# Kernel optimization log

Measured on AMD Instinct MI355X. Metric: run time of the kernel, lower is better.

The kernel has to match this reference:

```python
import jax, jax.numpy as jnp
import numpy as np

B, N, D, S = 16, 128, 128, 128   # batch, n_nodes, node/edge feat dim, state_dim
MP_INT = 256
UP_INT = 256
EPS = 1e-3  # keras BatchNormalization default epsilon


def _mlp(x, W1, b1, W2, b2):
    # Dense(relu) -> Dense(relu)
    h = jax.nn.relu(x @ W1 + b1)
    return jax.nn.relu(h @ W2 + b2)


def setup_inputs() -> dict:
    key = jax.random.key(0)
    ks = jax.random.split(key, 16)
    g = lambda k, shape: jax.random.normal(k, shape, dtype=jnp.float32) * 0.05
    nodes = jax.random.normal(ks[0], (B, N, D), dtype=jnp.float32)
    edges = jax.random.normal(ks[1], (B, N * N, D), dtype=jnp.float32)
    mask = (jax.random.uniform(ks[2], (B, N * N, 1)) > 0.5).astype(jnp.float32)
    return {
        "nodes": nodes, "edges": edges, "mask": mask,
        # Adj_Updater_1: concat(node_i, node_j, edge_ij) -> UP_INT -> S
        "W1a": g(ks[3], (3 * D, UP_INT)), "b1a": jnp.zeros((UP_INT,), jnp.float32),
        "W2a": g(ks[4], (UP_INT, S)), "b2a": jnp.zeros((S,), jnp.float32),
        # Message_Passer_1: concat(node_i, node_j, new_edge) -> MP_INT -> S
        "W1m": g(ks[5], (2 * D + S, MP_INT)), "b1m": jnp.zeros((MP_INT,), jnp.float32),
        "W2m": g(ks[6], (MP_INT, S)), "b2m": jnp.zeros((S,), jnp.float32),
        # Update_Func_1: concat(old_state, agg_messages) -> UP_INT -> S
        "W1u": g(ks[7], (D + S, UP_INT)), "b1u": jnp.zeros((UP_INT,), jnp.float32),
        "W2u": g(ks[8], (UP_INT, S)), "b2u": jnp.zeros((S,), jnp.float32),
        # BatchNorm (inference mode: moving stats) for nodes and edges
        "gamma_n": jnp.ones((S,), jnp.float32), "beta_n": jnp.zeros((S,), jnp.float32),
        "mean_n": jnp.zeros((S,), jnp.float32), "var_n": jnp.ones((S,), jnp.float32),
        "gamma_e": jnp.ones((S,), jnp.float32), "beta_e": jnp.zeros((S,), jnp.float32),
        "mean_e": jnp.zeros((S,), jnp.float32), "var_e": jnp.ones((S,), jnp.float32),
    }


def reference(nodes, edges, mask,
              W1a, b1a, W2a, b2a,
              W1m, b1m, W2m, b2m,
              W1u, b1u, W2u, b2u,
              gamma_n, beta_n, mean_n, var_n,
              gamma_e, beta_e, mean_e, var_e):
    b, n, d = nodes.shape
    # tf.tile(nodes,[1,n,1]): row p*n+q -> nodes[q]  (state_i)
    state_i = jnp.broadcast_to(nodes[:, None, :, :], (b, n, n, d)).reshape(b, n * n, d)
    # reshape(tile(nodes,[1,1,n])): row p*n+q -> nodes[p]  (state_j)
    state_j = jnp.broadcast_to(nodes[:, :, None, :], (b, n, n, d)).reshape(b, n * n, d)

    new_edges = _mlp(jnp.concatenate([state_i, state_j, edges], axis=-1), W1a, b1a, W2a, b2a)
    new_edges = new_edges * mask

    messages = _mlp(jnp.concatenate([state_i, state_j, new_edges], axis=-1), W1m, b1m, W2m, b2m)
    masked = (messages * mask).reshape(b, n, n, -1)
    agg_m = masked.sum(axis=2)  # reduce over axis 2 as in Message_Agg

    state_1 = _mlp(jnp.concatenate([nodes, agg_m], axis=-1), W1u, b1u, W2u, b2u)

    bn = lambda x, g_, b_, m_, v_: g_ * (x - m_) * jax.lax.rsqrt(v_ + EPS) + b_
    nodes_out = bn(state_1, gamma_n, beta_n, mean_n, var_n)
    edges_out = bn(new_edges, gamma_e, beta_e, mean_e, var_e)
    return nodes_out, edges_out
```

## Files before the change

### kernel.cpp

```cpp
#include <hip/hip_runtime.h>
#include <hip/hip_bf16.h>
#include <cstdint>
#include <cstddef>


typedef __attribute__((ext_vector_type(8))) __bf16 bf16x8;
typedef __attribute__((ext_vector_type(4))) float f32x4;

#define GLDS(gp, lp)                                                        \
  __builtin_amdgcn_global_load_lds(                                         \
      (const __attribute__((address_space(1))) void*)(gp),                  \
      (__attribute__((address_space(3))) void*)(lp), 16, 0, 0)

__device__ inline bf16x8 load8_cvt(const float* __restrict__ p) {
  const float4 a = *(const float4*)p;
  const float4 b = *(const float4*)(p + 4);
  bf16x8 r;
  r[0] = (__bf16)a.x; r[1] = (__bf16)a.y; r[2] = (__bf16)a.z; r[3] = (__bf16)a.w;
  r[4] = (__bf16)b.x; r[5] = (__bf16)b.y; r[6] = (__bf16)b.z; r[7] = (__bf16)b.w;
  return r;
}

__global__ void __launch_bounds__(256) proj_kernel(
    const float* __restrict__ nodes, const float* __restrict__ W1a,
    const float* __restrict__ b1a, const float* __restrict__ W1m,
    const float* __restrict__ b1m, const float* __restrict__ ge,
    const float* __restrict__ be, const float* __restrict__ me,
    const float* __restrict__ ve, float* __restrict__ outP) {
  __shared__ float x[8][128];
  const int mat = blockIdx.y;
  const int t = threadIdx.x;
  const float* W = (mat < 2 ? W1a : W1m) + ((mat & 1) ? 128 * 256 : 0);
  float* out = outP + (size_t)mat * (2048 * 256);
  const int r0 = blockIdx.x * 8;
  for (int i = t; i < 1024; i += 256)
    x[i >> 7][i & 127] = nodes[r0 * 128 + i];
  __syncthreads();
  float bv = 0.f;
  if (mat == 1) bv = b1a[t];
  if (mat == 3) {
    bv = b1m[t];
    const float* We = W1m + 65536;
    float cc = 0.f;
    for (int k = 0; k < 128; ++k) {
      float sc = ge[k] * rsqrtf(ve[k] + 1e-3f);
      float sh = be[k] - me[k] * sc;
      cc -= (sh / sc) * We[k * 256 + t];
    }
    bv += cc;
  }
  float acc[8];
#pragma unroll
  for (int r = 0; r < 8; ++r) acc[r] = bv;
  for (int k = 0; k < 128; ++k) {
    float w = W[k * 256 + t];
#pragma unroll
    for (int r = 0; r < 8; ++r) acc[r] += x[r][k] * w;
  }
  for (int r = 0; r < 8; ++r) out[(size_t)(r0 + r) * 256 + t] = acc[r];
}

__global__ void __launch_bounds__(256) wswz_kernel(
    const float* __restrict__ W1a, const float* __restrict__ W2a,
    const float* __restrict__ W1m, const float* __restrict__ W2m,
    const float* __restrict__ ge, const float* __restrict__ ve,
    __hip_bfloat16* __restrict__ dstp) {
  __bf16* dst = (__bf16*)dstp;
  const int mat = blockIdx.y;
  const float* src;
  __bf16* d;
  int nsh;
  if (mat == 0)      { src = W1a + 65536; d = dst;         nsh = 8; }
  else if (mat == 1) { src = W2a;         d = dst + 32768; nsh = 7; }
  else if (mat == 2) { src = W1m + 65536; d = dst + 65536; nsh = 8; }
  else               { src = W2m;         d = dst + 98304; nsh = 7; }
  const int nmask = (1 << nsh) - 1;
  const int base = (blockIdx.x * 256 + threadIdx.x) * 4;
#pragma unroll
  for (int i = 0; i < 4; ++i) {
    int s = base + i;
    int k = s >> nsh, n = s & nmask;
    float v = src[s];
    if (mat == 2) v *= sqrtf(ve[k] + 1e-3f) / ge[k];
    int g = k >> 3;
    if (nsh == 8) {
      int gs = (g & 8) | ((g ^ n) & 7);
      d[n * 128 + gs * 8 + (k & 7)] = (__bf16)v;
    } else {
      int gs = (g ^ n) & 7;
      d[((k >> 6) << 13) + (n << 6) + (gs << 3) + (k & 7)] = (__bf16)v;
    }
  }
}

__global__ void __launch_bounds__(256, 2) edge_mlp_kernel(
    const float* __restrict__ edges, const float* __restrict__ mask,
    const float* __restrict__ b2a, const float* __restrict__ ge,
    const float* __restrict__ be, const float* __restrict__ me,
    const float* __restrict__ ve, const float* __restrict__ Pa,
    const float* __restrict__ Qab, const __hip_bfloat16* __restrict__ Wsw,
    float* __restrict__ edges_out) {
  __shared__ __align__(16) char sW1h[16384];
  __shared__ __align__(16) char sW2h[16384];
  __shared__ __align__(16) char sH1q[16384];
  __shared__ float sQ[256];
  __shared__ float sB2[128];
  __shared__ float sMask[128];
  __shared__ float sScE[128];
  __shared__ float sShE[128];

  const int t = threadIdx.x;
  const int lane = t & 63, wv = t >> 6;
  const int cl = lane & 15, qd = lane >> 4;
  const int m0 = wv * 32;

  if (t < 128) {
    sB2[t] = b2a[t];
    float sc = ge[t] * rsqrtf(ve[t] + 1e-3f);
    sScE[t] = sc;
    sShE[t] = be[t] - me[t] * sc;
  }

  const int bb = blockIdx.x >> 5;
  const int p0 = (blockIdx.x & 31) * 4;
  const char* gW1base = (const char*)Wsw;
  const char* gW2base = (const char*)(Wsw + 32768);

  for (int tp = 0; tp < 4; ++tp) {
    const int p = p0 + tp;
    __syncthreads();
    sQ[t] = Qab[((bb << 7) + p) * 256 + t];
    if (t < 128) sMask[t] = mask[(bb << 14) + (p << 7) + t];

    const float* Xb = edges + ((size_t)((bb << 14) + (p << 7)) << 7);
    bf16x8 xf[2][4];
#pragma unroll
    for (int mt = 0; mt < 2; ++mt)
#pragma unroll
      for (int ks = 0; ks < 4; ++ks)
        xf[mt][ks] = load8_cvt(Xb + (m0 + mt * 16 + cl) * 128 + ks * 32 + qd * 8);

    f32x4 ne[2][8];
#pragma unroll
    for (int mt = 0; mt < 2; ++mt)
#pragma unroll
      for (int nt = 0; nt < 8; ++nt) {
        float bv = sB2[nt * 16 + cl];
        ne[mt][nt] = (f32x4){bv, bv, bv, bv};
      }

    for (int h = 0; h < 4; ++h) {
      __syncthreads();
      {
        const char* gW1 = gW1base + h * 16384;
        const char* gW2 = gW2base + h * 16384;
        for (int o = wv * 1024; o < 16384; o += 4096) {
          GLDS(gW1 + o + lane * 16, sW1h + o);
          GLDS(gW2 + o + lane * 16, sW2h + o);
        }
      }
      f32x4 a1[2][4];
#pragma unroll
      for (int mt = 0; mt < 2; ++mt)
#pragma unroll
        for (int nt = 0; nt < 4; ++nt) {
          const int col = h * 64 + nt * 16 + cl;
          const int mrow = m0 + mt * 16 + qd * 4;
          const float qv = sQ[col];
          const float* pa = Pa + (size_t)((bb << 7) + mrow) * 256 + col;
          a1[mt][nt] = (f32x4){pa[0] + qv, pa[256] + qv, pa[512] + qv, pa[768] + qv};
        }
      __syncthreads();
#pragma unroll
      for (int ks = 0; ks < 4; ++ks)
#pragma unroll
        for (int nt = 0; nt < 4; ++nt) {
          const int nl = nt * 16 + cl;
          const int g = ks * 4 + qd;
          const int gs = (g & 8) | ((g ^ nl) & 7);
          bf16x8 bw = *(const bf16x8*)(sW1h + nl * 256 + gs * 16);
          a1[0][nt] = __builtin_amdgcn_mfma_f32_16x16x32_bf16(xf[0][ks], bw, a1[0][nt], 0, 0, 0);
          a1[1][nt] = __builtin_amdgcn_mfma_f32_16x16x32_bf16(xf[1][ks], bw, a1[1][nt], 0, 0, 0);
        }
#pragma unroll
      for (int mt = 0; mt < 2; ++mt)
#pragma unroll
        for (int nt = 0; nt < 4; ++nt) {
          const int kq = nt * 16 + cl;
#pragma unroll
          for (int r = 0; r < 4; ++r) {
            const int m = m0 + mt * 16 + qd * 4 + r;
            float v = a1[mt][nt][r];
            v = v > 0.f ? v : 0.f;
            const int gs = ((kq >> 3) ^ m) & 7;
            *(__bf16*)(sH1q + m * 128 + gs * 16 + (kq & 7) * 2) = (__bf16)v;
          }
        }
      __syncthreads();
      bf16x8 hf[2][2];
#pragma unroll
      for (int mt = 0; mt < 2; ++mt)
#pragma unroll
        for (int ks = 0; ks < 2; ++ks) {
          const int m = m0 + mt * 16 + cl;
          const int g = ks * 4 + qd;
          const int gs = (g ^ m) & 7;
          hf[mt][ks] = *(const bf16x8*)(sH1q + m * 128 + gs * 16);
        }
#pragma unroll
      for (int ks = 0; ks < 2; ++ks)
#pragma unroll
        for (int nt = 0; nt < 8; ++nt) {
          const int n = nt * 16 + cl;
          const int g = ks * 4 + qd;
          const int gs = (g ^ n) & 7;
          bf16x8 bw = *(const bf16x8*)(sW2h + n * 128 + gs * 16);
          ne[0][nt] = __builtin_amdgcn_mfma_f32_16x16x32_bf16(hf[0][ks], bw, ne[0][nt], 0, 0, 0);
          ne[1][nt] = __builtin_amdgcn_mfma_f32_16x16x32_bf16(hf[1][ks], bw, ne[1][nt], 0, 0, 0);
        }
    }
    float* Ob = edges_out + ((size_t)((bb << 14) + (p << 7)) << 7);
#pragma unroll
    for (int mt = 0; mt < 2; ++mt)
#pragma unroll
      for (int nt = 0; nt < 8; ++nt) {
        const int col = nt * 16 + cl;
        const float sc = sScE[col], sh = sShE[col];
#pragma unroll
        for (int r = 0; r < 4; ++r) {
          const int m = m0 + mt * 16 + qd * 4 + r;
          float v = ne[mt][nt][r];
          v = v > 0.f ? v : 0.f;
          Ob[m * 128 + col] = (v * sMask[m]) * sc + sh;
        }
      }
  }
}

__global__ void __launch_bounds__(256, 2) msg_mlp_kernel(
    const float* __restrict__ mask, const float* __restrict__ b2m,
    const float* __restrict__ Pm, const float* __restrict__ Qmb,
    const __hip_bfloat16* __restrict__ Wsw, const float* __restrict__ Yedges,
    float* __restrict__ agg) {
  __shared__ __align__(16) char sW1h[16384];
  __shared__ __align__(16) char sW2h[16384];
  __shared__ __align__(16) char sH1q[16384];
  __shared__ float sQ[256];
  __shared__ float sB2[128];
  __shared__ float sMask[128];
  __shared__ float sAgg[512];

  const int t = threadIdx.x;
  const int lane = t & 63, wv = t >> 6;
  const int cl = lane & 15, qd = lane >> 4;
  const int m0 = wv * 32;

  if (t < 128) sB2[t] = b2m[t];

  const int bb = blockIdx.x >> 5;
  const int p0 = (blockIdx.x & 31) * 4;
  const char* gW1base = (const char*)Wsw;
  const char* gW2base = (const char*)(Wsw + 32768);

  for (int tp = 0; tp < 4; ++tp) {
    const int p = p0 + tp;
    __syncthreads();
    sQ[t] = Qmb[((bb << 7) + p) * 256 + t];
    if (t < 128) sMask[t] = mask[(bb << 14) + (p << 7) + t];

    const float* Xb = Yedges + ((size_t)((bb << 14) + (p << 7)) << 7);
    bf16x8 xf[2][4];
#pragma unroll
    for (int mt = 0; mt < 2; ++mt)
#pragma unroll
      for (int ks = 0; ks < 4; ++ks)
        xf[mt][ks] = load8_cvt(Xb + (m0 + mt * 16 + cl) * 128 + ks * 32 + qd * 8);

    f32x4 ms[2][8];
#pragma unroll
    for (int mt = 0; mt < 2; ++mt)
#pragma unroll
      for (int nt = 0; nt < 8; ++nt) {
        float bv = sB2[nt * 16 + cl];
        ms[mt][nt] = (f32x4){bv, bv, bv, bv};
      }

    for (int h = 0; h < 4; ++h) {
      __syncthreads();
      {
        const char* gW1 = gW1base + h * 16384;
        const char* gW2 = gW2base + h * 16384;
        for (int o = wv * 1024; o < 16384; o += 4096) {
          GLDS(gW1 + o + lane * 16, sW1h + o);
          GLDS(gW2 + o + lane * 16, sW2h + o);
        }
      }
      f32x4 a1[2][4];
#pragma unroll
      for (int mt = 0; mt < 2; ++mt)
#pragma unroll
        for (int nt = 0; nt < 4; ++nt) {
          const int col = h * 64 + nt * 16 + cl;
          const int mrow = m0 + mt * 16 + qd * 4;
          const float qv = sQ[col];
          const float* pa = Pm + (size_t)((bb << 7) + mrow) * 256 + col;
          a1[mt][nt] = (f32x4){pa[0] + qv, pa[256] + qv, pa[512] + qv, pa[768] + qv};
        }
      __syncthreads();
#pragma unroll
      for (int ks = 0; ks < 4; ++ks)
#pragma unroll
        for (int nt = 0; nt < 4; ++nt) {
          const int nl = nt * 16 + cl;
          const int g = ks * 4 + qd;
          const int gs = (g & 8) | ((g ^ nl) & 7);
          bf16x8 bw = *(const bf16x8*)(sW1h + nl * 256 + gs * 16);
          a1[0][nt] = __builtin_amdgcn_mfma_f32_16x16x32_bf16(xf[0][ks], bw, a1[0][nt], 0, 0, 0);
          a1[1][nt] = __builtin_amdgcn_mfma_f32_16x16x32_bf16(xf[1][ks], bw, a1[1][nt], 0, 0, 0);
        }
#pragma unroll
      for (int mt = 0; mt < 2; ++mt)
#pragma unroll
        for (int nt = 0; nt < 4; ++nt) {
          const int kq = nt * 16 + cl;
#pragma unroll
          for (int r = 0; r < 4; ++r) {
            const int m = m0 + mt * 16 + qd * 4 + r;
            float v = a1[mt][nt][r];
            v = v > 0.f ? v : 0.f;
            const int gs = ((kq >> 3) ^ m) & 7;
            *(__bf16*)(sH1q + m * 128 + gs * 16 + (kq & 7) * 2) = (__bf16)v;
          }
        }
      __syncthreads();
      bf16x8 hf[2][2];
#pragma unroll
      for (int mt = 0; mt < 2; ++mt)
#pragma unroll
        for (int ks = 0; ks < 2; ++ks) {
          const int m = m0 + mt * 16 + cl;
          const int g = ks * 4 + qd;
          const int gs = (g ^ m) & 7;
          hf[mt][ks] = *(const bf16x8*)(sH1q + m * 128 + gs * 16);
        }
#pragma unroll
      for (int ks = 0; ks < 2; ++ks)
#pragma unroll
        for (int nt = 0; nt < 8; ++nt) {
          const int n = nt * 16 + cl;
          const int g = ks * 4 + qd;
          const int gs = (g ^ n) & 7;
          bf16x8 bw = *(const bf16x8*)(sW2h + n * 128 + gs * 16);
          ms[0][nt] = __builtin_amdgcn_mfma_f32_16x16x32_bf16(hf[0][ks], bw, ms[0][nt], 0, 0, 0);
          ms[1][nt] = __builtin_amdgcn_mfma_f32_16x16x32_bf16(hf[1][ks], bw, ms[1][nt], 0, 0, 0);
        }
    }
#pragma unroll
    for (int nt = 0; nt < 8; ++nt) {
      float s = 0.f;
#pragma unroll
      for (int mt = 0; mt < 2; ++mt)
#pragma unroll
        for (int r = 0; r < 4; ++r) {
          const int m = m0 + mt * 16 + qd * 4 + r;
          float v = ms[mt][nt][r];
          v = v > 0.f ? v : 0.f;
          s += v * sMask[m];
        }
      s += __shfl_xor(s, 16);
      s += __shfl_xor(s, 32);
      if (lane < 16) sAgg[wv * 128 + nt * 16 + lane] = s;
    }
    __syncthreads();
    if (t < 128)
      agg[((bb << 7) + p) * 128 + t] =
          sAgg[t] + sAgg[128 + t] + sAgg[256 + t] + sAgg[384 + t];
  }
}

__global__ void __launch_bounds__(256) update_kernel(
    const float* __restrict__ nodes, const float* __restrict__ agg,
    const float* __restrict__ W1u, const float* __restrict__ b1u,
    const float* __restrict__ W2u, const float* __restrict__ b2u,
    const float* __restrict__ gn, const float* __restrict__ btn,
    const float* __restrict__ mn, const float* __restrict__ vn,
    float* __restrict__ out) {
  __shared__ float x[8][256];
  __shared__ float hh[8][256];
  const int t = threadIdx.x;
  const int r0 = blockIdx.x * 8;
  for (int i = t; i < 2048; i += 256) {
    int r = i >> 8, c = i & 255;
    x[r][c] = (c < 128) ? nodes[(r0 + r) * 128 + c] : agg[(r0 + r) * 128 + (c - 128)];
  }
  __syncthreads();
  float acc[8];
  {
    float bv = b1u[t];
#pragma unroll
    for (int r = 0; r < 8; ++r) acc[r] = bv;
  }
  for (int k = 0; k < 256; ++k) {
    float w = W1u[k * 256 + t];
#pragma unroll
    for (int r = 0; r < 8; ++r) acc[r] += x[r][k] * w;
  }
#pragma unroll
  for (int r = 0; r < 8; ++r) hh[r][t] = acc[r] > 0.f ? acc[r] : 0.f;
  __syncthreads();
  const int j = t & 127, half = t >> 7;
  float a2[4];
  {
    float bv = b2u[j];
#pragma unroll
    for (int r = 0; r < 4; ++r) a2[r] = bv;
  }
  for (int k = 0; k < 256; ++k) {
    float w = W2u[k * 128 + j];
#pragma unroll
    for (int r = 0; r < 4; ++r) a2[r] += hh[half * 4 + r][k] * w;
  }
  float sc = gn[j] * rsqrtf(vn[j] + 1e-3f);
  float sh = btn[j] - mn[j] * sc;
#pragma unroll
  for (int r = 0; r < 4; ++r) {
    float v = a2[r] > 0.f ? a2[r] : 0.f;
    out[(r0 + half * 4 + r) * 128 + j] = v * sc + sh;
  }
}

extern "C" void kernel_launch(void* const* d_in, const int* in_sizes, int n_in,
                              void* d_out, int out_size, void* d_ws,
                              size_t ws_size, hipStream_t stream) {
  (void)in_sizes; (void)n_in; (void)out_size; (void)ws_size;
  const float* nodes = (const float*)d_in[0];
  const float* edges = (const float*)d_in[1];
  const float* mask = (const float*)d_in[2];
  const float* W1a = (const float*)d_in[3];
  const float* b1a = (const float*)d_in[4];
  const float* W2a = (const float*)d_in[5];
  const float* b2a = (const float*)d_in[6];
  const float* W1m = (const float*)d_in[7];
  const float* b1m = (const float*)d_in[8];
  const float* W2m = (const float*)d_in[9];
  const float* b2m = (const float*)d_in[10];
  const float* W1u = (const float*)d_in[11];
  const float* b1u = (const float*)d_in[12];
  const float* W2u = (const float*)d_in[13];
  const float* b2u = (const float*)d_in[14];
  const float* gn = (const float*)d_in[15];
  const float* btn = (const float*)d_in[16];
  const float* mn = (const float*)d_in[17];
  const float* vn = (const float*)d_in[18];
  const float* ge = (const float*)d_in[19];
  const float* be = (const float*)d_in[20];
  const float* me = (const float*)d_in[21];
  const float* ve = (const float*)d_in[22];

  float* out_nodes = (float*)d_out;
  float* out_edges = (float*)d_out + 262144;

  char* ws = (char*)d_ws;
  float* Pa = (float*)(ws);
  float* Qab = (float*)(ws + ((size_t)1 << 21));
  float* Pm = (float*)(ws + ((size_t)2 << 21));
  float* Qmb = (float*)(ws + ((size_t)3 << 21));
  float* agg = (float*)(ws + ((size_t)4 << 21));
  __hip_bfloat16* Wsw = (__hip_bfloat16*)(ws + ((size_t)4 << 21) + ((size_t)1 << 20));

  proj_kernel<<<dim3(256, 4), 256, 0, stream>>>(nodes, W1a, b1a, W1m, b1m, ge,
                                                be, me, ve, Pa);
  wswz_kernel<<<dim3(32, 4), 256, 0, stream>>>(W1a, W2a, W1m, W2m, ge, ve, Wsw);
  edge_mlp_kernel<<<512, 256, 0, stream>>>(edges, mask, b2a, ge, be, me, ve, Pa,
                                           Qab, Wsw, out_edges);
  msg_mlp_kernel<<<512, 256, 0, stream>>>(mask, b2m, Pm, Qmb, Wsw + 65536,
                                          out_edges, agg);
  update_kernel<<<256, 256, 0, stream>>>(nodes, agg, W1u, b1u, W2u, b2u, gn, btn,
                                         mn, vn, out_nodes);
}
```

Baseline: 452.7 us.

## Merge prep kernels and give each edge/message block one node row

```diff
diff --git a/kernel.cpp b/kernel.cpp
--- a/kernel.cpp
+++ b/kernel.cpp
@@ -21,15 +21,45 @@
   return r;
 }
 
-__global__ void __launch_bounds__(256) proj_kernel(
+__global__ void __launch_bounds__(256) prep_kernel(
     const float* __restrict__ nodes, const float* __restrict__ W1a,
     const float* __restrict__ b1a, const float* __restrict__ W1m,
-    const float* __restrict__ b1m, const float* __restrict__ ge,
+    const float* __restrict__ b1m, const float* __restrict__ W2a,
+    const float* __restrict__ W2m, const float* __restrict__ ge,
     const float* __restrict__ be, const float* __restrict__ me,
-    const float* __restrict__ ve, float* __restrict__ outP) {
-  __shared__ float x[8][128];
+    const float* __restrict__ ve, float* __restrict__ outP,
+    __hip_bfloat16* __restrict__ dstp) {
   const int mat = blockIdx.y;
   const int t = threadIdx.x;
+  if (blockIdx.x >= 256) {
+    __bf16* dst = (__bf16*)dstp;
+    const float* src;
+    __bf16* d;
+    int nsh;
+    if (mat == 0)      { src = W1a + 65536; d = dst;         nsh = 8; }
+    else if (mat == 1) { src = W2a;         d = dst + 32768; nsh = 7; }
+    else if (mat == 2) { src = W1m + 65536; d = dst + 65536; nsh = 8; }
+    else               { src = W2m;         d = dst + 98304; nsh = 7; }
+    const int nmask = (1 << nsh) - 1;
+    const int base = ((blockIdx.x - 256) * 256 + t) * 4;
+#pragma unroll
+    for (int i = 0; i < 4; ++i) {
+      int s = base + i;
+      int k = s >> nsh, n = s & nmask;
+      float v = src[s];
+      if (mat == 2) v *= sqrtf(ve[k] + 1e-3f) / ge[k];
+      int g = k >> 3;
+      if (nsh == 8) {
+        int gs = (g & 8) | ((g ^ n) & 7);
+        d[n * 128 + gs * 8 + (k & 7)] = (__bf16)v;
+      } else {
+        int gs = (g ^ n) & 7;
+        d[((k >> 6) << 13) + (n << 6) + (gs << 3) + (k & 7)] = (__bf16)v;
+      }
+    }
+    return;
+  }
+  __shared__ float x[8][128];
   const float* W = (mat < 2 ? W1a : W1m) + ((mat & 1) ? 128 * 256 : 0);
   float* out = outP + (size_t)mat * (2048 * 256);
   const int r0 = blockIdx.x * 8;
@@ -60,40 +90,7 @@
   for (int r = 0; r < 8; ++r) out[(size_t)(r0 + r) * 256 + t] = acc[r];
 }
 
-__global__ void __launch_bounds__(256) wswz_kernel(
-    const float* __restrict__ W1a, const float* __restrict__ W2a,
-    const float* __restrict__ W1m, const float* __restrict__ W2m,
-    const float* __restrict__ ge, const float* __restrict__ ve,
-    __hip_bfloat16* __restrict__ dstp) {
-  __bf16* dst = (__bf16*)dstp;
-  const int mat = blockIdx.y;
-  const float* src;
-  __bf16* d;
-  int nsh;
-  if (mat == 0)      { src = W1a + 65536; d = dst;         nsh = 8; }
-  else if (mat == 1) { src = W2a;         d = dst + 32768; nsh = 7; }
-  else if (mat == 2) { src = W1m + 65536; d = dst + 65536; nsh = 8; }
-  else               { src = W2m;         d = dst + 98304; nsh = 7; }
-  const int nmask = (1 << nsh) - 1;
-  const int base = (blockIdx.x * 256 + threadIdx.x) * 4;
-#pragma unroll
-  for (int i = 0; i < 4; ++i) {
-    int s = base + i;
-    int k = s >> nsh, n = s & nmask;
-    float v = src[s];
-    if (mat == 2) v *= sqrtf(ve[k] + 1e-3f) / ge[k];
-    int g = k >> 3;
-    if (nsh == 8) {
-      int gs = (g & 8) | ((g ^ n) & 7);
-      d[n * 128 + gs * 8 + (k & 7)] = (__bf16)v;
-    } else {
-      int gs = (g ^ n) & 7;
-      d[((k >> 6) << 13) + (n << 6) + (gs << 3) + (k & 7)] = (__bf16)v;
-    }
-  }
-}
-
-__global__ void __launch_bounds__(256, 2) edge_mlp_kernel(
+__global__ void __launch_bounds__(256, 3) edge_mlp_kernel(
     const float* __restrict__ edges, const float* __restrict__ mask,
     const float* __restrict__ b2a, const float* __restrict__ ge,
     const float* __restrict__ be, const float* __restrict__ me,
@@ -114,130 +111,128 @@
   const int cl = lane & 15, qd = lane >> 4;
   const int m0 = wv * 32;
 
+  const int bb = blockIdx.x >> 7;
+  const int p = blockIdx.x & 127;
+
   if (t < 128) {
     sB2[t] = b2a[t];
     float sc = ge[t] * rsqrtf(ve[t] + 1e-3f);
     sScE[t] = sc;
     sShE[t] = be[t] - me[t] * sc;
-  }
-
-  const int bb = blockIdx.x >> 5;
-  const int p0 = (blockIdx.x & 31) * 4;
+    sMask[t] = mask[(bb << 14) + (p << 7) + t];
+  }
+  sQ[t] = Qab[((bb << 7) + p) * 256 + t];
+
+  const float* Xb = edges + ((size_t)((bb << 14) + (p << 7)) << 7);
+  bf16x8 xf[2][4];
+#pragma unroll
+  for (int mt = 0; mt < 2; ++mt)
+#pragma unroll
+    for (int ks = 0; ks < 4; ++ks)
+      xf[mt][ks] = load8_cvt(Xb + (m0 + mt * 16 + cl) * 128 + ks * 32 + qd * 8);
+
   const char* gW1base = (const char*)Wsw;
   const char* gW2base = (const char*)(Wsw + 32768);
 
-  for (int tp = 0; tp < 4; ++tp) {
-    const int p = p0 + tp;
+  __syncthreads();
+
+  f32x4 ne[2][8];
+#pragma unroll
+  for (int mt = 0; mt < 2; ++mt)
+#pragma unroll
+    for (int nt = 0; nt < 8; ++nt) {
+      float bv = sB2[nt * 16 + cl];
+      ne[mt][nt] = (f32x4){bv, bv, bv, bv};
+    }
+
+  for (int h = 0; h < 4; ++h) {
+    if (h) __syncthreads();
+    {
+      const char* gW1 = gW1base + h * 16384;
+      const char* gW2 = gW2base + h * 16384;
+      for (int o = wv * 1024; o < 16384; o += 4096) {
+        GLDS(gW1 + o + lane * 16, sW1h + o);
+        GLDS(gW2 + o + lane * 16, sW2h + o);
+      }
+    }
+    f32x4 a1[2][4];
+#pragma unroll
+    for (int mt = 0; mt < 2; ++mt)
+#pragma unroll
+      for (int nt = 0; nt < 4; ++nt) {
+        const int col = h * 64 + nt * 16 + cl;
+        const int mrow = m0 + mt * 16 + qd * 4;
+        const float qv = sQ[col];
+        const float* pa = Pa + (size_t)((bb << 7) + mrow) * 256 + col;
+        a1[mt][nt] = (f32x4){pa[0] + qv, pa[256] + qv, pa[512] + qv, pa[768] + qv};
+      }
     __syncthreads();
-    sQ[t] = Qab[((bb << 7) + p) * 256 + t];
-    if (t < 128) sMask[t] = mask[(bb << 14) + (p << 7) + t];
-
-    const float* Xb = edges + ((size_t)((bb << 14) + (p << 7)) << 7);
-    bf16x8 xf[2][4];
-#pragma unroll
-    for (int mt = 0; mt < 2; ++mt)
-#pragma unroll
-      for (int ks = 0; ks < 4; ++ks)
-        xf[mt][ks] = load8_cvt(Xb + (m0 + mt * 16 + cl) * 128 + ks * 32 + qd * 8);
-
-    f32x4 ne[2][8];
-#pragma unroll
-    for (int mt = 0; mt < 2; ++mt)
-#pragma unroll
-      for (int nt = 0; nt < 8; ++nt) {
-        float bv = sB2[nt * 16 + cl];
-        ne[mt][nt] = (f32x4){bv, bv, bv, bv};
-      }
-
-    for (int h = 0; h < 4; ++h) {
-      __syncthreads();
-      {
-        const char* gW1 = gW1base + h * 16384;
-        const char* gW2 = gW2base + h * 16384;
-        for (int o = wv * 1024; o < 16384; o += 4096) {
-          GLDS(gW1 + o + lane * 16, sW1h + o);
-          GLDS(gW2 + o + lane * 16, sW2h + o);
-        }
-      }
-      f32x4 a1[2][4];
-#pragma unroll
-      for (int mt = 0; mt < 2; ++mt)
-#pragma unroll
-        for (int nt = 0; nt < 4; ++nt) {
-          const int col = h * 64 + nt * 16 + cl;
-          const int mrow = m0 + mt * 16 + qd * 4;
-          const float qv = sQ[col];
-          const float* pa = Pa + (size_t)((bb << 7) + mrow) * 256 + col;
-          a1[mt][nt] = (f32x4){pa[0] + qv, pa[256] + qv, pa[512] + qv, pa[768] + qv};
-        }
-      __syncthreads();
-#pragma unroll
-      for (int ks = 0; ks < 4; ++ks)
-#pragma unroll
-        for (int nt = 0; nt < 4; ++nt) {
-          const int nl = nt * 16 + cl;
-          const int g = ks * 4 + qd;
-          const int gs = (g & 8) | ((g ^ nl) & 7);
-          bf16x8 bw = *(const bf16x8*)(sW1h + nl * 256 + gs * 16);
-          a1[0][nt] = __builtin_amdgcn_mfma_f32_16x16x32_bf16(xf[0][ks], bw, a1[0][nt], 0, 0, 0);
-          a1[1][nt] = __builtin_amdgcn_mfma_f32_16x16x32_bf16(xf[1][ks], bw, a1[1][nt], 0, 0, 0);
-        }
-#pragma unroll
-      for (int mt = 0; mt < 2; ++mt)
-#pragma unroll
-        for (int nt = 0; nt < 4; ++nt) {
-          const int kq = nt * 16 + cl;
-#pragma unroll
-          for (int r = 0; r < 4; ++r) {
-            const int m = m0 + mt * 16 + qd * 4 + r;
-            float v = a1[mt][nt][r];
-            v = v > 0.f ? v : 0.f;
-            const int gs = ((kq >> 3) ^ m) & 7;
-            *(__bf16*)(sH1q + m * 128 + gs * 16 + (kq & 7) * 2) = (__bf16)v;
-          }
-        }
-      __syncthreads();
-      bf16x8 hf[2][2];
-#pragma unroll
-      for (int mt = 0; mt < 2; ++mt)
-#pragma unroll
-        for (int ks = 0; ks < 2; ++ks) {
-          const int m = m0 + mt * 16 + cl;
-          const int g = ks * 4 + qd;
-          const int gs = (g ^ m) & 7;
-          hf[mt][ks] = *(const bf16x8*)(sH1q + m * 128 + gs * 16);
-        }
-#pragma unroll
-      for (int ks = 0; ks < 2; ++ks)
-#pragma unroll
-        for (int nt = 0; nt < 8; ++nt) {
-          const int n = nt * 16 + cl;
-          const int g = ks * 4 + qd;
-          const int gs = (g ^ n) & 7;
-          bf16x8 bw = *(const bf16x8*)(sW2h + n * 128 + gs * 16);
-          ne[0][nt] = __builtin_amdgcn_mfma_f32_16x16x32_bf16(hf[0][ks], bw, ne[0][nt], 0, 0, 0);
-          ne[1][nt] = __builtin_amdgcn_mfma_f32_16x16x32_bf16(hf[1][ks], bw, ne[1][nt], 0, 0, 0);
-        }
-    }
-    float* Ob = edges_out + ((size_t)((bb << 14) + (p << 7)) << 7);
-#pragma unroll
-    for (int mt = 0; mt < 2; ++mt)
-#pragma unroll
-      for (int nt = 0; nt < 8; ++nt) {
-        const int col = nt * 16 + cl;
-        const float sc = sScE[col], sh = sShE[col];
+#pragma unroll
+    for (int ks = 0; ks < 4; ++ks)
+#pragma unroll
+      for (int nt = 0; nt < 4; ++nt) {
+        const int nl = nt * 16 + cl;
+        const int g = ks * 4 + qd;
+        const int gs = (g & 8) | ((g ^ nl) & 7);
+        bf16x8 bw = *(const bf16x8*)(sW1h + nl * 256 + gs * 16);
+        a1[0][nt] = __builtin_amdgcn_mfma_f32_16x16x32_bf16(xf[0][ks], bw, a1[0][nt], 0, 0, 0);
+        a1[1][nt] = __builtin_amdgcn_mfma_f32_16x16x32_bf16(xf[1][ks], bw, a1[1][nt], 0, 0, 0);
+      }
+#pragma unroll
+    for (int mt = 0; mt < 2; ++mt)
+#pragma unroll
+      for (int nt = 0; nt < 4; ++nt) {
+        const int kq = nt * 16 + cl;
 #pragma unroll
         for (int r = 0; r < 4; ++r) {
           const int m = m0 + mt * 16 + qd * 4 + r;
-          float v = ne[mt][nt][r];
+          float v = a1[mt][nt][r];
           v = v > 0.f ? v : 0.f;
-          Ob[m * 128 + col] = (v * sMask[m]) * sc + sh;
+          const int gs = ((kq >> 3) ^ m) & 7;
+          *(__bf16*)(sH1q + m * 128 + gs * 16 + (kq & 7) * 2) = (__bf16)v;
         }
       }
-  }
-}
-
-__global__ void __launch_bounds__(256, 2) msg_mlp_kernel(
+    __syncthreads();
+    bf16x8 hf[2][2];
+#pragma unroll
+    for (int mt = 0; mt < 2; ++mt)
+#pragma unroll
+      for (int ks = 0; ks < 2; ++ks) {
+        const int m = m0 + mt * 16 + cl;
+        const int g = ks * 4 + qd;
+        const int gs = (g ^ m) & 7;
+        hf[mt][ks] = *(const bf16x8*)(sH1q + m * 128 + gs * 16);
+      }
+#pragma unroll
+    for (int ks = 0; ks < 2; ++ks)
+#pragma unroll
+      for (int nt = 0; nt < 8; ++nt) {
+        const int n = nt * 16 + cl;
+        const int g = ks * 4 + qd;
+        const int gs = (g ^ n) & 7;
+        bf16x8 bw = *(const bf16x8*)(sW2h + n * 128 + gs * 16);
+        ne[0][nt] = __builtin_amdgcn_mfma_f32_16x16x32_bf16(hf[0][ks], bw, ne[0][nt], 0, 0, 0);
+        ne[1][nt] = __builtin_amdgcn_mfma_f32_16x16x32_bf16(hf[1][ks], bw, ne[1][nt], 0, 0, 0);
+      }
+  }
+  float* Ob = edges_out + ((size_t)((bb << 14) + (p << 7)) << 7);
+#pragma unroll
+  for (int mt = 0; mt < 2; ++mt)
+#pragma unroll
+    for (int nt = 0; nt < 8; ++nt) {
+      const int col = nt * 16 + cl;
+      const float sc = sScE[col], sh = sShE[col];
+#pragma unroll
+      for (int r = 0; r < 4; ++r) {
+        const int m = m0 + mt * 16 + qd * 4 + r;
+        float v = ne[mt][nt][r];
+        v = v > 0.f ? v : 0.f;
+        Ob[m * 128 + col] = (v * sMask[m]) * sc + sh;
+      }
+    }
+}
+
+__global__ void __launch_bounds__(256, 3) msg_mlp_kernel(
     const float* __restrict__ mask, const float* __restrict__ b2m,
     const float* __restrict__ Pm, const float* __restrict__ Qmb,
     const __hip_bfloat16* __restrict__ Wsw, const float* __restrict__ Yedges,
@@ -255,127 +250,127 @@
   const int cl = lane & 15, qd = lane >> 4;
   const int m0 = wv * 32;
 
-  if (t < 128) sB2[t] = b2m[t];
-
-  const int bb = blockIdx.x >> 5;
-  const int p0 = (blockIdx.x & 31) * 4;
+  const int bb = blockIdx.x >> 7;
+  const int p = blockIdx.x & 127;
+
+  if (t < 128) {
+    sB2[t] = b2m[t];
+    sMask[t] = mask[(bb << 14) + (p << 7) + t];
+  }
+  sQ[t] = Qmb[((bb << 7) + p) * 256 + t];
+
+  const float* Xb = Yedges + ((size_t)((bb << 14) + (p << 7)) << 7);
+  bf16x8 xf[2][4];
+#pragma unroll
+  for (int mt = 0; mt < 2; ++mt)
+#pragma unroll
+    for (int ks = 0; ks < 4; ++ks)
+      xf[mt][ks] = load8_cvt(Xb + (m0 + mt * 16 + cl) * 128 + ks * 32 + qd * 8);
+
   const char* gW1base = (const char*)Wsw;
   const char* gW2base = (const char*)(Wsw + 32768);
 
-  for (int tp = 0; tp < 4; ++tp) {
-    const int p = p0 + tp;
+  __syncthreads();
+
+  f32x4 ms[2][8];
+#pragma unroll
+  for (int mt = 0; mt < 2; ++mt)
+#pragma unroll
+    for (int nt = 0; nt < 8; ++nt) {
+      float bv = sB2[nt * 16 + cl];
+      ms[mt][nt] = (f32x4){bv, bv, bv, bv};
+    }
+
+  for (int h = 0; h < 4; ++h) {
+    if (h) __syncthreads();
+    {
+      const char* gW1 = gW1base + h * 16384;
+      const char* gW2 = gW2base + h * 16384;
+      for (int o = wv * 1024; o < 16384; o += 4096) {
+        GLDS(gW1 + o + lane * 16, sW1h + o);
+        GLDS(gW2 + o + lane * 16, sW2h + o);
+      }
+    }
+    f32x4 a1[2][4];
+#pragma unroll
+    for (int mt = 0; mt < 2; ++mt)
+#pragma unroll
+      for (int nt = 0; nt < 4; ++nt) {
+        const int col = h * 64 + nt * 16 + cl;
+        const int mrow = m0 + mt * 16 + qd * 4;
+        const float qv = sQ[col];
+        const float* pa = Pm + (size_t)((bb << 7) + mrow) * 256 + col;
+        a1[mt][nt] = (f32x4){pa[0] + qv, pa[256] + qv, pa[512] + qv, pa[768] + qv};
+      }
     __syncthreads();
-    sQ[t] = Qmb[((bb << 7) + p) * 256 + t];
-    if (t < 128) sMask[t] = mask[(bb << 14) + (p << 7) + t];
-
-    const float* Xb = Yedges + ((size_t)((bb << 14) + (p << 7)) << 7);
-    bf16x8 xf[2][4];
-#pragma unroll
-    for (int mt = 0; mt < 2; ++mt)
-#pragma unroll
-      for (int ks = 0; ks < 4; ++ks)
-        xf[mt][ks] = load8_cvt(Xb + (m0 + mt * 16 + cl) * 128 + ks * 32 + qd * 8);
-
-    f32x4 ms[2][8];
-#pragma unroll
-    for (int mt = 0; mt < 2; ++mt)
-#pragma unroll
-      for (int nt = 0; nt < 8; ++nt) {
-        float bv = sB2[nt * 16 + cl];
-        ms[mt][nt] = (f32x4){bv, bv, bv, bv};
-      }
-
-    for (int h = 0; h < 4; ++h) {
-      __syncthreads();
-      {
-        const char* gW1 = gW1base + h * 16384;
-        const char* gW2 = gW2base + h * 16384;
-        for (int o = wv * 1024; o < 16384; o += 4096) {
-          GLDS(gW1 + o + lane * 16, sW1h + o);
-          GLDS(gW2 + o + lane * 16, sW2h + o);
-        }
-      }
-      f32x4 a1[2][4];
-#pragma unroll
-      for (int mt = 0; mt < 2; ++mt)
-#pragma unroll
-        for (int nt = 0; nt < 4; ++nt) {
-          const int col = h * 64 + nt * 16 + cl;
-          const int mrow = m0 + mt * 16 + qd * 4;
-          const float qv = sQ[col];
-          const float* pa = Pm + (size_t)((bb << 7) + mrow) * 256 + col;
-          a1[mt][nt] = (f32x4){pa[0] + qv, pa[256] + qv, pa[512] + qv, pa[768] + qv};
-        }
-      __syncthreads();
-#pragma unroll
-      for (int ks = 0; ks < 4; ++ks)
-#pragma unroll
-        for (int nt = 0; nt < 4; ++nt) {
-          const int nl = nt * 16 + cl;
-          const int g = ks * 4 + qd;
-          const int gs = (g & 8) | ((g ^ nl) & 7);
-          bf16x8 bw = *(const bf16x8*)(sW1h + nl * 256 + gs * 16);
-          a1[0][nt] = __builtin_amdgcn_mfma_f32_16x16x32_bf16(xf[0][ks], bw, a1[0][nt], 0, 0, 0);
-          a1[1][nt] = __builtin_amdgcn_mfma_f32_16x16x32_bf16(xf[1][ks], bw, a1[1][nt], 0, 0, 0);
-        }
-#pragma unroll
-      for (int mt = 0; mt < 2; ++mt)
-#pragma unroll
-        for (int nt = 0; nt < 4; ++nt) {
-          const int kq = nt * 16 + cl;
-#pragma unroll
-          for (int r = 0; r < 4; ++r) {
-            const int m = m0 + mt * 16 + qd * 4 + r;
-            float v = a1[mt][nt][r];
-            v = v > 0.f ? v : 0.f;
-            const int gs = ((kq >> 3) ^ m) & 7;
-            *(__bf16*)(sH1q + m * 128 + gs * 16 + (kq & 7) * 2) = (__bf16)v;
-          }
-        }
-      __syncthreads();
-      bf16x8 hf[2][2];
-#pragma unroll
-      for (int mt = 0; mt < 2; ++mt)
-#pragma unroll
-        for (int ks = 0; ks < 2; ++ks) {
-          const int m = m0 + mt * 16 + cl;
-          const int g = ks * 4 + qd;
-          const int gs = (g ^ m) & 7;
-          hf[mt][ks] = *(const bf16x8*)(sH1q + m * 128 + gs * 16);
-        }
-#pragma unroll
-      for (int ks = 0; ks < 2; ++ks)
-#pragma unroll
-        for (int nt = 0; nt < 8; ++nt) {
-          const int n = nt * 16 + cl;
-          const int g = ks * 4 + qd;
-          const int gs = (g ^ n) & 7;
-          bf16x8 bw = *(const bf16x8*)(sW2h + n * 128 + gs * 16);
-          ms[0][nt] = __builtin_amdgcn_mfma_f32_16x16x32_bf16(hf[0][ks], bw, ms[0][nt], 0, 0, 0);
-          ms[1][nt] = __builtin_amdgcn_mfma_f32_16x16x32_bf16(hf[1][ks], bw, ms[1][nt], 0, 0, 0);
-        }
-    }
-#pragma unroll
-    for (int nt = 0; nt < 8; ++nt) {
-      float s = 0.f;
-#pragma unroll
-      for (int mt = 0; mt < 2; ++mt)
+#pragma unroll
+    for (int ks = 0; ks < 4; ++ks)
+#pragma unroll
+      for (int nt = 0; nt < 4; ++nt) {
+        const int nl = nt * 16 + cl;
+        const int g = ks * 4 + qd;
+        const int gs = (g & 8) | ((g ^ nl) & 7);
+        bf16x8 bw = *(const bf16x8*)(sW1h + nl * 256 + gs * 16);
+        a1[0][nt] = __builtin_amdgcn_mfma_f32_16x16x32_bf16(xf[0][ks], bw, a1[0][nt], 0, 0, 0);
+        a1[1][nt] = __builtin_amdgcn_mfma_f32_16x16x32_bf16(xf[1][ks], bw, a1[1][nt], 0, 0, 0);
+      }
+#pragma unroll
+    for (int mt = 0; mt < 2; ++mt)
+#pragma unroll
+      for (int nt = 0; nt < 4; ++nt) {
+        const int kq = nt * 16 + cl;
 #pragma unroll
         for (int r = 0; r < 4; ++r) {
           const int m = m0 + mt * 16 + qd * 4 + r;
-          float v = ms[mt][nt][r];
+          float v = a1[mt][nt][r];
           v = v > 0.f ? v : 0.f;
-          s += v * sMask[m];
+          const int gs = ((kq >> 3) ^ m) & 7;
+          *(__bf16*)(sH1q + m * 128 + gs * 16 + (kq & 7) * 2) = (__bf16)v;
         }
-      s += __shfl_xor(s, 16);
-      s += __shfl_xor(s, 32);
-      if (lane < 16) sAgg[wv * 128 + nt * 16 + lane] = s;
-    }
+      }
     __syncthreads();
-    if (t < 128)
-      agg[((bb << 7) + p) * 128 + t] =
-          sAgg[t] + sAgg[128 + t] + sAgg[256 + t] + sAgg[384 + t];
-  }
+    bf16x8 hf[2][2];
+#pragma unroll
+    for (int mt = 0; mt < 2; ++mt)
+#pragma unroll
+      for (int ks = 0; ks < 2; ++ks) {
+        const int m = m0 + mt * 16 + cl;
+        const int g = ks * 4 + qd;
+        const int gs = (g ^ m) & 7;
+        hf[mt][ks] = *(const bf16x8*)(sH1q + m * 128 + gs * 16);
+      }
+#pragma unroll
+    for (int ks = 0; ks < 2; ++ks)
+#pragma unroll
+      for (int nt = 0; nt < 8; ++nt) {
+        const int n = nt * 16 + cl;
+        const int g = ks * 4 + qd;
+        const int gs = (g ^ n) & 7;
+        bf16x8 bw = *(const bf16x8*)(sW2h + n * 128 + gs * 16);
+        ms[0][nt] = __builtin_amdgcn_mfma_f32_16x16x32_bf16(hf[0][ks], bw, ms[0][nt], 0, 0, 0);
+        ms[1][nt] = __builtin_amdgcn_mfma_f32_16x16x32_bf16(hf[1][ks], bw, ms[1][nt], 0, 0, 0);
+      }
+  }
+#pragma unroll
+  for (int nt = 0; nt < 8; ++nt) {
+    float s = 0.f;
+#pragma unroll
+    for (int mt = 0; mt < 2; ++mt)
+#pragma unroll
+      for (int r = 0; r < 4; ++r) {
+        const int m = m0 + mt * 16 + qd * 4 + r;
+        float v = ms[mt][nt][r];
+        v = v > 0.f ? v : 0.f;
+        s += v * sMask[m];
+      }
+    s += __shfl_xor(s, 16);
+    s += __shfl_xor(s, 32);
+    if (lane < 16) sAgg[wv * 128 + nt * 16 + lane] = s;
+  }
+  __syncthreads();
+  if (t < 128)
+    agg[((bb << 7) + p) * 128 + t] =
+        sAgg[t] + sAgg[128 + t] + sAgg[256 + t] + sAgg[384 + t];
 }
 
 __global__ void __launch_bounds__(256) update_kernel(
@@ -468,13 +463,12 @@
   float* agg = (float*)(ws + ((size_t)4 << 21));
   __hip_bfloat16* Wsw = (__hip_bfloat16*)(ws + ((size_t)4 << 21) + ((size_t)1 << 20));
 
-  proj_kernel<<<dim3(256, 4), 256, 0, stream>>>(nodes, W1a, b1a, W1m, b1m, ge,
-                                                be, me, ve, Pa);
-  wswz_kernel<<<dim3(32, 4), 256, 0, stream>>>(W1a, W2a, W1m, W2m, ge, ve, Wsw);
-  edge_mlp_kernel<<<512, 256, 0, stream>>>(edges, mask, b2a, ge, be, me, ve, Pa,
-                                           Qab, Wsw, out_edges);
-  msg_mlp_kernel<<<512, 256, 0, stream>>>(mask, b2m, Pm, Qmb, Wsw + 65536,
-                                          out_edges, agg);
+  prep_kernel<<<dim3(288, 4), 256, 0, stream>>>(nodes, W1a, b1a, W1m, b1m, W2a,
+                                                W2m, ge, be, me, ve, Pa, Wsw);
+  edge_mlp_kernel<<<2048, 256, 0, stream>>>(edges, mask, b2a, ge, be, me, ve,
+                                            Pa, Qab, Wsw, out_edges);
+  msg_mlp_kernel<<<2048, 256, 0, stream>>>(mask, b2m, Pm, Qmb, Wsw + 65536,
+                                           out_edges, agg);
   update_kernel<<<256, 256, 0, stream>>>(nodes, agg, W1u, b1u, W2u, b2u, gn, btn,
                                          mn, vn, out_nodes);
 }
```

Result: slower. 546.9 us (+20.8%).
